# Kernel optimization log

Hardware: AMD Instinct MI355X
Metric: run time of the kernel (lower is better)

The kernel has to match this reference:

```python
import jax, jax.numpy as jnp
import numpy as np

U, D_IN, RANK, N = 128, 10240, 320, 32

def setup_inputs() -> dict:
    key = jax.random.key(0)
    ks = jax.random.split(key, 9)
    s = 0.02
    return {
        "x": jax.random.normal(ks[0], (U, D_IN), jnp.float32),
        "h": jax.random.normal(ks[1], (U, D_IN, N), jnp.float32),
        "W_delta": jax.random.normal(ks[2], (D_IN, RANK), jnp.float32) * s,
        "W_dt": jax.random.normal(ks[3], (RANK, D_IN), jnp.float32) * s,
        "b_dt": jax.random.normal(ks[4], (D_IN,), jnp.float32) * s,
        "W_B": jax.random.normal(ks[5], (D_IN, N), jnp.float32) * s,
        "W_C": jax.random.normal(ks[6], (D_IN, N), jnp.float32) * s,
        # A = -exp(A_log): strictly negative, so exp(delta*A) in (0,1)
        "A": -jnp.exp(jax.random.normal(ks[7], (D_IN, N), jnp.float32) * 0.5),
        "D": jax.random.normal(ks[8], (D_IN,), jnp.float32),
    }

def reference(x, h, W_delta, W_dt, b_dt, W_B, W_C, A, D):
    # dt projection: low-rank then up-proj + bias, softplus (beta=1, threshold=20)
    delta = jax.nn.softplus(x @ W_delta @ W_dt + b_dt)          # [U, D_IN]
    # B and C input-dependent projections
    B = x @ W_B                                                  # [U, N]
    C = x @ W_C                                                  # [U, N]
    # discretize: abar = exp(delta * A); bbar*x = delta * B * x
    abar = jnp.exp(delta[:, :, None] * A[None, :, :])            # [U, D_IN, N]
    bx = (delta * x)[:, :, None] * B[:, None, :]                 # [U, D_IN, N]
    h_new = abar * h + bx                                        # state update
    # output: y_d = sum_n h[d,n] * C[n] + D_d * x_d
    y = jnp.einsum('udn,un->ud', h_new, C) + D[None, :] * x      # [U, D_IN]
    return y, h_new
```

## Files before the change

### kernel.cpp

```cpp
#include <hip/hip_runtime.h>

#define U_    128
#define DIN   10240
#define RANK  320
#define NS    32
#define NTOT  384
#define KC    32
#define KCH   (DIN / KC)

__global__ __launch_bounds__(256) void transpose_kernel(
    const float* __restrict__ x, float* __restrict__ xT)
{
    __shared__ float tile[32][33];
    int kb = blockIdx.x * 32, ub = blockIdx.y * 32;
    int tx = threadIdx.x, ty = threadIdx.y;
#pragma unroll
    for (int i = 0; i < 32; i += 8)
        tile[ty + i][tx] = x[(size_t)(ub + ty + i) * DIN + kb + tx];
    __syncthreads();
#pragma unroll
    for (int i = 0; i < 32; i += 8)
        xT[(size_t)(kb + ty + i) * U_ + ub + tx] = tile[tx][ty + i];
}

__global__ __launch_bounds__(64) void gemmA_kernel(
    const float* __restrict__ xT,
    const float* __restrict__ Wd, const float* __restrict__ Wb,
    const float* __restrict__ Wc,
    float* __restrict__ partial)
{
    int b  = blockIdx.x;
    int uh = b & 1;
    int nt = (b >> 1) % 12;
    int kc = b / 24;
    int u  = uh * 64 + threadIdx.x;
    int n0 = nt * 32;

    const float* W; int ldw, c0;
    if (nt < 10)       { W = Wd; ldw = RANK; c0 = n0; }
    else if (nt == 10) { W = Wb; ldw = NS;   c0 = 0;  }
    else               { W = Wc; ldw = NS;   c0 = 0;  }

    float acc[32];
#pragma unroll
    for (int j = 0; j < 32; ++j) acc[j] = 0.f;

    int k0 = kc * KCH;
    const float* Wp = W  + (size_t)k0 * ldw + c0;
    const float* xp = xT + (size_t)k0 * U_ + u;

#pragma unroll 2
    for (int k = 0; k < KCH; ++k) {
        float xv = xp[(size_t)k * U_];
#pragma unroll
        for (int j = 0; j < 32; ++j)
            acc[j] += xv * Wp[(size_t)k * ldw + j];
    }

    float* out = partial + (size_t)kc * (NTOT * U_) + (size_t)n0 * U_ + u;
#pragma unroll
    for (int j = 0; j < 32; ++j)
        out[(size_t)j * U_] = acc[j];
}

__global__ __launch_bounds__(256) void reduce_kernel(
    const float* __restrict__ partial, float* __restrict__ tT,
    float* __restrict__ Bc, float* __restrict__ Cc)
{
    int e = blockIdx.x * 256 + threadIdx.x;
    float s = 0.f;
#pragma unroll 8
    for (int kc = 0; kc < KC; ++kc)
        s += partial[(size_t)kc * (NTOT * U_) + e];
    int n = e >> 7, u = e & 127;
    if (n < RANK)            tT[e] = s;
    else if (n < RANK + NS)  Bc[u * NS + (n - RANK)] = s;
    else                     Cc[u * NS + (n - RANK - NS)] = s;
}

__global__ __launch_bounds__(64) void delta_kernel(
    const float* __restrict__ tT, const float* __restrict__ Wdt,
    const float* __restrict__ b_dt, float* __restrict__ delta)
{
    int b  = blockIdx.x;
    int dt_ = b % 160, ut = b / 160;
    int d  = dt_ * 64 + threadIdx.x;
    int u0 = ut * 32;

    float bias = b_dt[d];
    float acc[32];
#pragma unroll
    for (int i = 0; i < 32; ++i) acc[i] = bias;

#pragma unroll 2
    for (int r = 0; r < RANK; ++r) {
        float w = Wdt[(size_t)r * DIN + d];
        const float* tp = tT + r * U_ + u0;
#pragma unroll
        for (int i = 0; i < 32; ++i)
            acc[i] += w * tp[i];
    }
#pragma unroll
    for (int i = 0; i < 32; ++i) {
        float z = acc[i];
        float sp = (z > 20.f) ? z : log1pf(__expf(z));
        delta[(size_t)(u0 + i) * DIN + d] = sp;
    }
}

__global__ __launch_bounds__(256) void ssm_kernel(
    const float* __restrict__ x, const float* __restrict__ h,
    const float* __restrict__ delta,
    const float* __restrict__ Bc, const float* __restrict__ Cc,
    const float* __restrict__ A, const float* __restrict__ Dvec,
    float* __restrict__ y, float* __restrict__ hnew)
{
    int idx4 = blockIdx.x * 256 + threadIdx.x;
    int n4 = idx4 & 7;
    int ud = idx4 >> 3;
    int d = ud % DIN;
    int u = ud / DIN;

    float dlt = delta[ud];
    float xv  = x[ud];

    float4 hv = ((const float4*)h)[idx4];
    float4 av = ((const float4*)A)[(size_t)d * 8 + n4];
    float4 bv = ((const float4*)Bc)[u * 8 + n4];
    float4 cv = ((const float4*)Cc)[u * 8 + n4];

    float dx = dlt * xv;
    float4 hn;
    hn.x = __expf(dlt * av.x) * hv.x + dx * bv.x;
    hn.y = __expf(dlt * av.y) * hv.y + dx * bv.y;
    hn.z = __expf(dlt * av.z) * hv.z + dx * bv.z;
    hn.w = __expf(dlt * av.w) * hv.w + dx * bv.w;

    ((float4*)hnew)[idx4] = hn;

    float p = hn.x * cv.x + hn.y * cv.y + hn.z * cv.z + hn.w * cv.w;
    p += __shfl_xor(p, 4, 8);
    p += __shfl_xor(p, 2, 8);
    p += __shfl_xor(p, 1, 8);
    if (n4 == 0)
        y[ud] = p + Dvec[d] * xv;
}

extern "C" void kernel_launch(void* const* d_in, const int* in_sizes, int n_in,
                              void* d_out, int out_size, void* d_ws, size_t ws_size,
                              hipStream_t stream)
{
    const float* x   = (const float*)d_in[0];
    const float* h   = (const float*)d_in[1];
    const float* Wd  = (const float*)d_in[2];
    const float* Wdt = (const float*)d_in[3];
    const float* bdt = (const float*)d_in[4];
    const float* Wb  = (const float*)d_in[5];
    const float* Wc  = (const float*)d_in[6];
    const float* A   = (const float*)d_in[7];
    const float* Dv  = (const float*)d_in[8];

    float* ws      = (float*)d_ws;
    float* xT      = ws;
    float* partial = ws + 1310720;
    float* delta   = partial;
    float* tT      = ws + 1310720 + 1572864;
    float* Bc      = tT + 40960;
    float* Cc      = Bc + 4096;

    float* y    = (float*)d_out;
    float* hnew = y + (size_t)U_ * DIN;

    dim3 tb(32, 8);
    transpose_kernel<<<dim3(DIN / 32, U_ / 32), tb, 0, stream>>>(x, xT);
    gemmA_kernel    <<<768, 64, 0, stream>>>(xT, Wd, Wb, Wc, partial);
    reduce_kernel   <<<192, 256, 0, stream>>>(partial, tT, Bc, Cc);
    delta_kernel    <<<640, 64, 0, stream>>>(tT, Wdt, bdt, delta);
    ssm_kernel      <<<40960, 256, 0, stream>>>(x, h, delta, Bc, Cc, A, Dv, y, hnew);
}
```

Baseline: 481.7 us.

## Retile both projection GEMMs as 4x4 register-blocked float4 thread tiles

Both small GEMMs (x·[Wd|Wb|Wc] and t·Wdt) move from one-thread-per-row with 32 scalar accumulators to 256-thread blocks where each thread computes a 4x4 tile from float4 loads of both operands. This cuts per-thread register pressure and turns broadcast scalar weight loads into vectorized coalesced loads, which should raise occupancy and memory efficiency. Block counts drop (384 and 320 blocks), which may reduce parallelism on a many-CU GPU. The ssm kernel, which handles the large h stream, is unchanged, so the end-to-end effect is limited to the GEMM stages.

New measurement: 508.4 us. 5.5% more time.

```diff
diff --git a/kernel.cpp b/kernel.cpp
--- a/kernel.cpp
+++ b/kernel.cpp
@@ -7,6 +7,10 @@
 #define NTOT  384
 #define KC    32
 #define KCH   (DIN / KC)
+
+__device__ __forceinline__ void fma4(float4& a, const float4& v, float s) {
+    a.x += v.x * s; a.y += v.y * s; a.z += v.z * s; a.w += v.w * s;
+}
 
 __global__ __launch_bounds__(256) void transpose_kernel(
     const float* __restrict__ x, float* __restrict__ xT)
@@ -23,44 +27,44 @@
         xT[(size_t)(kb + ty + i) * U_ + ub + tx] = tile[tx][ty + i];
 }
 
-__global__ __launch_bounds__(64) void gemmA_kernel(
+__global__ __launch_bounds__(256) void gemm1_kernel(
     const float* __restrict__ xT,
     const float* __restrict__ Wd, const float* __restrict__ Wb,
     const float* __restrict__ Wc,
     float* __restrict__ partial)
 {
     int b  = blockIdx.x;
-    int uh = b & 1;
-    int nt = (b >> 1) % 12;
-    int kc = b / 24;
-    int u  = uh * 64 + threadIdx.x;
-    int n0 = nt * 32;
+    int nt = b % 12;
+    int kc = b / 12;
+    int ug = threadIdx.x & 31;
+    int ng = threadIdx.x >> 5;
 
-    const float* W; int ldw, c0;
-    if (nt < 10)       { W = Wd; ldw = RANK; c0 = n0; }
-    else if (nt == 10) { W = Wb; ldw = NS;   c0 = 0;  }
-    else               { W = Wc; ldw = NS;   c0 = 0;  }
-
-    float acc[32];
-#pragma unroll
-    for (int j = 0; j < 32; ++j) acc[j] = 0.f;
+    const float* W; int ldw, c0, nbase;
+    if (nt < 10)       { W = Wd; ldw = RANK; c0 = nt * 32; nbase = nt * 32; }
+    else if (nt == 10) { W = Wb; ldw = NS;   c0 = 0;       nbase = 320;     }
+    else               { W = Wc; ldw = NS;   c0 = 0;       nbase = 352;     }
 
     int k0 = kc * KCH;
-    const float* Wp = W  + (size_t)k0 * ldw + c0;
-    const float* xp = xT + (size_t)k0 * U_ + u;
+    const float* xp = xT + (size_t)k0 * U_ + 4 * ug;
+    const float* wp = W  + (size_t)k0 * ldw + c0 + 4 * ng;
 
-#pragma unroll 2
+    float4 acc0 = {0,0,0,0}, acc1 = {0,0,0,0}, acc2 = {0,0,0,0}, acc3 = {0,0,0,0};
+
+#pragma unroll 8
     for (int k = 0; k < KCH; ++k) {
-        float xv = xp[(size_t)k * U_];
-#pragma unroll
-        for (int j = 0; j < 32; ++j)
-            acc[j] += xv * Wp[(size_t)k * ldw + j];
+        float4 xv = *(const float4*)(xp + (size_t)k * U_);
+        float4 wv = *(const float4*)(wp + (size_t)k * ldw);
+        fma4(acc0, xv, wv.x);
+        fma4(acc1, xv, wv.y);
+        fma4(acc2, xv, wv.z);
+        fma4(acc3, xv, wv.w);
     }
 
-    float* out = partial + (size_t)kc * (NTOT * U_) + (size_t)n0 * U_ + u;
-#pragma unroll
-    for (int j = 0; j < 32; ++j)
-        out[(size_t)j * U_] = acc[j];
+    float* out = partial + ((size_t)kc * NTOT + nbase + 4 * ng) * U_ + 4 * ug;
+    *(float4*)(out)          = acc0;
+    *(float4*)(out + U_)     = acc1;
+    *(float4*)(out + 2 * U_) = acc2;
+    *(float4*)(out + 3 * U_) = acc3;
 }
 
 __global__ __launch_bounds__(256) void reduce_kernel(
@@ -78,33 +82,42 @@
     else                     Cc[u * NS + (n - RANK - NS)] = s;
 }
 
-__global__ __launch_bounds__(64) void delta_kernel(
+__global__ __launch_bounds__(256) void gemm2_kernel(
     const float* __restrict__ tT, const float* __restrict__ Wdt,
     const float* __restrict__ b_dt, float* __restrict__ delta)
 {
-    int b  = blockIdx.x;
-    int dt_ = b % 160, ut = b / 160;
-    int d  = dt_ * 64 + threadIdx.x;
-    int u0 = ut * 32;
+    int b   = blockIdx.x;
+    int dt_ = b % 80, ut = b / 80;
+    int dg = threadIdx.x & 31, ug = threadIdx.x >> 5;
+    int d0 = dt_ * 128 + 4 * dg;
+    int u0 = ut * 32 + 4 * ug;
 
-    float bias = b_dt[d];
-    float acc[32];
+    float4 bias = *(const float4*)(b_dt + d0);
+    float4 acc0 = bias, acc1 = bias, acc2 = bias, acc3 = bias;
+
+    const float* wp = Wdt + d0;
+    const float* tp = tT + u0;
+
+#pragma unroll 8
+    for (int r = 0; r < RANK; ++r) {
+        float4 wv = *(const float4*)(wp + (size_t)r * DIN);
+        float4 tv = *(const float4*)(tp + (size_t)r * U_);
+        fma4(acc0, wv, tv.x);
+        fma4(acc1, wv, tv.y);
+        fma4(acc2, wv, tv.z);
+        fma4(acc3, wv, tv.w);
+    }
+
+    float4 a[4] = {acc0, acc1, acc2, acc3};
 #pragma unroll
-    for (int i = 0; i < 32; ++i) acc[i] = bias;
-
-#pragma unroll 2
-    for (int r = 0; r < RANK; ++r) {
-        float w = Wdt[(size_t)r * DIN + d];
-        const float* tp = tT + r * U_ + u0;
-#pragma unroll
-        for (int i = 0; i < 32; ++i)
-            acc[i] += w * tp[i];
-    }
-#pragma unroll
-    for (int i = 0; i < 32; ++i) {
-        float z = acc[i];
-        float sp = (z > 20.f) ? z : log1pf(__expf(z));
-        delta[(size_t)(u0 + i) * DIN + d] = sp;
+    for (int i = 0; i < 4; ++i) {
+        float4 z = a[i];
+        float4 sp;
+        sp.x = (z.x > 20.f) ? z.x : log1pf(__expf(z.x));
+        sp.y = (z.y > 20.f) ? z.y : log1pf(__expf(z.y));
+        sp.z = (z.z > 20.f) ? z.z : log1pf(__expf(z.z));
+        sp.w = (z.w > 20.f) ? z.w : log1pf(__expf(z.w));
+        *(float4*)(delta + (size_t)(u0 + i) * DIN + d0) = sp;
     }
 }
 
@@ -173,8 +186,8 @@
 
     dim3 tb(32, 8);
     transpose_kernel<<<dim3(DIN / 32, U_ / 32), tb, 0, stream>>>(x, xT);
-    gemmA_kernel    <<<768, 64, 0, stream>>>(xT, Wd, Wb, Wc, partial);
+    gemm1_kernel    <<<384, 256, 0, stream>>>(xT, Wd, Wb, Wc, partial);
     reduce_kernel   <<<192, 256, 0, stream>>>(partial, tT, Bc, Cc);
-    delta_kernel    <<<640, 64, 0, stream>>>(tT, Wdt, bdt, delta);
+    gemm2_kernel    <<<320, 256, 0, stream>>>(tT, Wdt, bdt, delta);
     ssm_kernel      <<<40960, 256, 0, stream>>>(x, h, delta, Bc, Cc, A, Dv, y, hnew);
 }
```
